# Performance work log

Hardware: AMD Instinct MI355X
Metric: run time of the kernel (lower is better)

## Reference

```python
import jax, jax.numpy as jnp
import numpy as np

B, T, DM, H, D = 2, 4096, 1024, 16, 64
HD = H * D
PHASE_SCALE = 10.0


def _multiscale_phasors(num_heads, head_dim):
    # Deterministic multiscale frequencies: RoPE-like geometric spacing over
    # the feature dim, with a per-head octave scale (reconstruction of the
    # registered buffer `freqs` from generate_multiscale_phasors).
    d = np.arange(head_dim, dtype=np.float32) / head_dim
    base = 10000.0 ** (-d)                      # (D,)
    head_scale = 2.0 ** (-np.arange(num_heads, dtype=np.float32))  # (H,)
    return jnp.asarray(2.0 * np.pi * head_scale[:, None] * base[None, :],
                       dtype=jnp.float32)       # (H, D)


def setup_inputs() -> dict:
    key = jax.random.key(0)
    k0, k1, k2, k3 = jax.random.split(key, 4)
    x = jax.random.normal(k0, (B, T, DM), jnp.float32)
    Wk = jax.random.normal(k1, (DM, HD), jnp.float32) / np.float32(np.sqrt(DM))
    Wv = jax.random.normal(k2, (DM, HD), jnp.float32) / np.float32(np.sqrt(DM))
    Wo = jax.random.normal(k3, (HD, DM), jnp.float32) / np.float32(np.sqrt(HD))
    gate = jnp.full((H, 2), 0.5, jnp.float32)
    freqs = _multiscale_phasors(H, D)
    return {"x": x, "Wk": Wk, "Wv": Wv, "Wo": Wo, "gate": gate, "freqs": freqs}


def _holo_fused_step(v, binder, probe):
    # (cumsum(v * binder, dim=1) * probe).real / sqrt(1..T)
    mem = jnp.cumsum(v * binder, axis=1)                     # (B,T,H,D) complex64
    t = v.shape[1]
    scale = jnp.sqrt(jnp.arange(1, t + 1, dtype=jnp.float32))[None, :, None, None]
    return jnp.real(mem * probe) / scale                     # (B,T,H,D) float32


def reference(x, Wk, Wv, Wo, gate, freqs):
    Bb, Tt, _ = x.shape
    k_real = (x @ Wk).reshape(Bb, Tt, H, D)                  # (B,T,H,D)
    v = (x @ Wv).reshape(Bb, Tt, H, D).astype(jnp.complex64)
    k = jnp.exp(1j * (k_real * PHASE_SCALE))                 # unit phasors, q = k
    # Positional path: rotors = exp(i * t * freqs)
    t = jnp.arange(Tt, dtype=jnp.float32)
    rotors = jnp.exp(1j * (t[:, None, None] * freqs))[None]  # (1,T,H,D)
    out_pos = _holo_fused_step(v, rotors, jnp.conj(rotors))
    # Associative path: bind with conj of shifted keys, retrieve with q=k
    k_shifted = jnp.roll(k, 1, axis=1).at[:, 0].set(0.0)
    out_assoc = _holo_fused_step(v, jnp.conj(k_shifted), k)
    g_pos = gate[:, 0][None, None, :, None]
    g_assoc = gate[:, 1][None, None, :, None]
    out = out_pos * g_pos + out_assoc * g_assoc              # (B,T,H,D)
    return out.reshape(Bb, Tt, HD) @ Wo                      # dropout p=0 -> identity
```

## Files before the change

### kernel.cpp

```cpp
#include <hip/hip_runtime.h>


#define B_ 2
#define T_ 4096
#define H_ 16
#define D_ 64
#define M_ (B_*T_)
#define PHASE_SCALE 10.0f

typedef _Float16 f16;
typedef unsigned int u32;
typedef __attribute__((ext_vector_type(8))) _Float16 f16x8;
typedef __attribute__((ext_vector_type(4))) _Float16 f16x4;
typedef __attribute__((ext_vector_type(4))) float f32x4;


__global__ void k_prep(const float* __restrict__ x, const float* __restrict__ Wk,
                       const float* __restrict__ Wv, const float* __restrict__ Wo,
                       f16* __restrict__ xh, f16* __restrict__ Wkvt, f16* __restrict__ Wot) {
  __shared__ float tile[32][33];
  const int z = blockIdx.z;
  const int tx = threadIdx.x, ty = threadIdx.y;
  if (z == 3) {
    const int blk = blockIdx.y * 32 + blockIdx.x;
    const size_t base = (size_t)blk * 256 + ty * 32 + tx;
    #pragma unroll
    for (int i = 0; i < 8; ++i) {
      size_t idx = (base + (size_t)i * 262144) * 4;
      float4 v = *reinterpret_cast<const float4*>(x + idx);
      f16x4 o; o[0] = (f16)v.x; o[1] = (f16)v.y; o[2] = (f16)v.z; o[3] = (f16)v.w;
      *reinterpret_cast<f16x4*>(xh + idx) = o;
    }
    return;
  }
  const float* src = (z == 0) ? Wk : (z == 1) ? Wv : Wo;
  f16* dst = (z == 0) ? Wkvt : (z == 1) ? (Wkvt + (size_t)1024 * 1024) : Wot;
  const int bx = blockIdx.x, by = blockIdx.y;
  #pragma unroll
  for (int r = 0; r < 32; r += 8)
    tile[ty + r][tx] = src[(size_t)(by * 32 + ty + r) * 1024 + bx * 32 + tx];
  __syncthreads();
  #pragma unroll
  for (int r = 0; r < 32; r += 8)
    dst[(size_t)(bx * 32 + ty + r) * 1024 + by * 32 + tx] = (f16)tile[tx][ty + r];
}


__device__ __forceinline__ void gl2lds16(const f16* g, char* l) {
  __builtin_amdgcn_global_load_lds((const __attribute__((address_space(1))) u32*)g,
                                   (__attribute__((address_space(3))) u32*)l, 16, 0, 0);
}

#define S_BAR() __builtin_amdgcn_s_barrier()
#define WAIT_LGKM0() do { asm volatile("s_waitcnt lgkmcnt(0)" ::: "memory"); \
                          __builtin_amdgcn_sched_barrier(0); } while (0)
#define WAIT_VM(n) asm volatile("s_waitcnt vmcnt(" #n ")" ::: "memory")

#define STAGE_A(gp, ldsoff, kkt) do { \
  gl2lds16((gp) + (size_t)(kkt) * 64, smem + (ldsoff) + tid * 16); \
  if constexpr (MI == 4) \
    gl2lds16((gp) + (size_t)(kkt) * 64 + 64 * 1024, smem + (ldsoff) + 8192 + tid * 16); \
} while (0)
#define STAGE_B(gp, ldsoff, kkt) do { \
  gl2lds16((gp) + (size_t)(kkt) * 64, smem + (ldsoff) + tid * 16); \
  gl2lds16((gp) + (size_t)(kkt) * 64 + 64 * 1024, smem + (ldsoff) + 8192 + tid * 16); \
} while (0)

#define PHASE(AH, BH, READ_A, READ_B, VMW, STG) do { \
  if (READ_A) { \
    _Pragma("unroll") for (int mi = 0; mi < MI; ++mi) \
    _Pragma("unroll") for (int kk = 0; kk < 2; ++kk) \
      aF[mi][kk] = *(const f16x8*)(smem + curbuf + (AH) * AHB + offA[mi][kk]); \
  } \
  if (READ_B) { \
    _Pragma("unroll") for (int nj = 0; nj < 2; ++nj) \
    _Pragma("unroll") for (int kk = 0; kk < 2; ++kk) \
      bF[BH][nj][kk] = *(const f16x8*)(smem + curbuf + 2 * AHB + (BH) * 16384 + offB[nj][kk]); \
  } \
  STG; \
  S_BAR(); \
  WAIT_LGKM0(); \
  __builtin_amdgcn_s_setprio(1); \
  _Pragma("unroll") for (int mi = 0; mi < MI; ++mi) \
  _Pragma("unroll") for (int nj = 0; nj < 2; ++nj) \
  _Pragma("unroll") for (int kk = 0; kk < 2; ++kk) \
    acc[(AH) * 2 + (BH)][mi][nj] = __builtin_amdgcn_mfma_f32_16x16x32_f16( \
        aF[mi][kk], bF[BH][nj][kk], acc[(AH) * 2 + (BH)][mi][nj], 0, 0, 0); \
  __builtin_amdgcn_s_setprio(0); \
  VMW; \
  S_BAR(); \
} while (0)

template<int MI>
__launch_bounds__(512, 1)
__global__ void k_gemm8(const f16* __restrict__ A, const f16* __restrict__ Bt,
                        float* __restrict__ C32, f16* __restrict__ C16) {
  extern __shared__ char smem[];
  constexpr int AH_R = MI * 32;
  constexpr int AHB  = AH_R * 128;
  constexpr int BUFSZ = 2 * AHB + 32768;
  const int tid  = threadIdx.x;
  const int lane = tid & 63;
  const int wid  = tid >> 6;
  const int wr   = wid >> 2, wc = wid & 3;
  const int lr   = lane & 15, hi = lane >> 4;
  const int m0   = blockIdx.x * (MI * 64);
  const int n0   = blockIdx.y * 256;

  const int rsub = tid >> 3;
  const int csw  = ((tid & 7) ^ (rsub & 7)) * 8;
  const f16* gA0 = A  + (size_t)(m0 + rsub) * 1024 + csw;
  const f16* gA1 = gA0 + (size_t)AH_R * 1024;
  const f16* gB0 = Bt + (size_t)(n0 + rsub) * 1024 + csw;
  const f16* gB1 = gB0 + (size_t)128 * 1024;

  int offA[MI][2], offB[2][2];
  #pragma unroll
  for (int mi = 0; mi < MI; ++mi)
    #pragma unroll
    for (int kk = 0; kk < 2; ++kk) {
      int row = wr * (MI * 16) + mi * 16 + lr;
      offA[mi][kk] = row * 128 + (((kk * 4 + hi) ^ (row & 7)) << 4);
    }
  #pragma unroll
  for (int nj = 0; nj < 2; ++nj)
    #pragma unroll
    for (int kk = 0; kk < 2; ++kk) {
      int row = wc * 32 + nj * 16 + lr;
      offB[nj][kk] = row * 128 + (((kk * 4 + hi) ^ (row & 7)) << 4);
    }

  f32x4 acc[4][MI][2] = {};
  f16x8 aF[MI][2], bF[2][2][2];

  STAGE_A(gA0, 0,            0);
  STAGE_B(gB0, 2 * AHB,      0);
  STAGE_A(gA1, AHB,          0);
  STAGE_A(gA0, BUFSZ,        1);
  STAGE_B(gB1, 2 * AHB + 16384, 0);
  STAGE_B(gB0, BUFSZ + 2 * AHB, 1);
  if constexpr (MI == 4) WAIT_VM(8); else WAIT_VM(6);
  S_BAR();

  for (int kt = 0; kt < 14; ++kt) {
    const int curbuf = (kt & 1) * BUFSZ;
    const int nxtbuf = curbuf ^ BUFSZ;
    PHASE(0, 0, 1, 1, if constexpr (MI == 4) WAIT_VM(4); else WAIT_VM(3),
          STAGE_A(gA1, nxtbuf + AHB, kt + 1));
    PHASE(0, 1, 0, 1, (void)0, STAGE_A(gA0, curbuf, kt + 2));
    PHASE(1, 0, 1, 0, (void)0, STAGE_B(gB1, nxtbuf + 2 * AHB + 16384, kt + 1));
    PHASE(1, 1, 0, 0, if constexpr (MI == 4) WAIT_VM(8); else WAIT_VM(6),
          STAGE_B(gB0, curbuf + 2 * AHB, kt + 2));
  }
  {
    const int curbuf = 0, nxtbuf = BUFSZ;
    PHASE(0, 0, 1, 1, if constexpr (MI == 4) WAIT_VM(4); else WAIT_VM(3),
          STAGE_A(gA1, nxtbuf + AHB, 15));
    PHASE(0, 1, 0, 1, (void)0, (void)0);
    PHASE(1, 0, 1, 0, (void)0, STAGE_B(gB1, nxtbuf + 2 * AHB + 16384, 15));
    PHASE(1, 1, 0, 0, if constexpr (MI == 4) WAIT_VM(4); else WAIT_VM(3), (void)0);
  }
  {
    const int curbuf = BUFSZ;
    PHASE(0, 0, 1, 1, WAIT_VM(0), (void)0);
    PHASE(0, 1, 0, 1, (void)0, (void)0);
    PHASE(1, 0, 1, 0, (void)0, (void)0);
    PHASE(1, 1, 0, 0, (void)0, (void)0);
  }

  const int rb = hi * 4;
  #pragma unroll
  for (int ah = 0; ah < 2; ++ah)
    #pragma unroll
    for (int bh = 0; bh < 2; ++bh)
      #pragma unroll
      for (int mi = 0; mi < MI; ++mi)
        #pragma unroll
        for (int nj = 0; nj < 2; ++nj) {
          f32x4 a4 = acc[ah * 2 + bh][mi][nj];
          const int row = m0 + ah * AH_R + wr * (MI * 16) + mi * 16 + rb;
          const int col = n0 + bh * 128 + wc * 32 + nj * 16 + lr;
          if (col < 1024) {
            #pragma unroll
            for (int r = 0; r < 4; ++r)
              C32[(size_t)(row + r) * 1024 + col] = a4[r];
          } else {
            #pragma unroll
            for (int r = 0; r < 4; ++r)
              C16[(size_t)(row + r) * 1024 + (col - 1024)] = (f16)a4[r];
          }
        }
}


__global__ void k_scan_part(const float* __restrict__ kf, const f16* __restrict__ vh,
                            const float* __restrict__ freqs, float4* __restrict__ tot) {
  const int bid = blockIdx.x;
  const int cg = bid & 15;
  const int h  = (bid >> 4) & 15;
  const int b  = bid >> 8;
  const int w  = threadIdx.x >> 6;
  const int d  = threadIdx.x & 63;
  const int c  = cg * 4 + w;
  const int t0 = c * 64;
  const int col = h * 64 + d;
  const float f = freqs[col];

  float bc = 0.f, bs = 0.f;
  if (t0 > 0) {
    float krp = kf[(size_t)(b * T_ + t0 - 1) * 1024 + col];
    __sincosf(PHASE_SCALE * krp, &bs, &bc);
  }
  double rev = (double)t0 * (double)f * 0.15915494309189535;
  rev -= floor(rev);
  float ph = (float)rev * 6.28318530717958647692f;
  float ri, rc; __sincosf(ph, &ri, &rc);
  float sf, cf; __sincosf(f, &sf, &cf);

  float pr = 0.f, pi = 0.f, ar = 0.f, ai = 0.f;
  #pragma unroll 4
  for (int tt = 0; tt < 64; ++tt) {
    size_t row = (size_t)(b * T_ + t0 + tt) * 1024 + col;
    float v  = (float)vh[row];
    float kr = kf[row];
    pr = fmaf(v, rc, pr); pi = fmaf(v, ri, pi);
    ar = fmaf(v, bc, ar); ai = fmaf(-v, bs, ai);
    __sincosf(PHASE_SCALE * kr, &bs, &bc);
    float nrc = rc * cf - ri * sf;
    ri = rc * sf + ri * cf; rc = nrc;
  }
  tot[((size_t)(c * 2 + b) * 16 + h) * 64 + d] = make_float4(pr, pi, ar, ai);
}

__global__ void k_scan_out(const float* __restrict__ kf, const f16* __restrict__ vh,
                           const float* __restrict__ freqs, const float4* __restrict__ tot,
                           const float* __restrict__ gate, f16* __restrict__ y) {
  const int bid = blockIdx.x;
  const int cg = bid & 15;
  const int h  = (bid >> 4) & 15;
  const int b  = bid >> 8;
  const int w  = threadIdx.x >> 6;
  const int d  = threadIdx.x & 63;
  const int c  = cg * 4 + w;
  const int t0 = c * 64;
  const int col = h * 64 + d;
  const float f = freqs[col];
  const float gp = gate[2 * h], ga = gate[2 * h + 1];

  float pr = 0.f, pi = 0.f, ar = 0.f, ai = 0.f;
  for (int cc = 0; cc < c; ++cc) {
    float4 tv = tot[((size_t)(cc * 2 + b) * 16 + h) * 64 + d];
    pr += tv.x; pi += tv.y; ar += tv.z; ai += tv.w;
  }

  float bc = 0.f, bs = 0.f;
  if (t0 > 0) {
    float krp = kf[(size_t)(b * T_ + t0 - 1) * 1024 + col];
    __sincosf(PHASE_SCALE * krp, &bs, &bc);
  }
  double rev = (double)t0 * (double)f * 0.15915494309189535;
  rev -= floor(rev);
  float ph = (float)rev * 6.28318530717958647692f;
  float ri, rc; __sincosf(ph, &ri, &rc);
  float sf, cf; __sincosf(f, &sf, &cf);

  #pragma unroll 4
  for (int tt = 0; tt < 64; ++tt) {
    int t = t0 + tt;
    size_t row = (size_t)(b * T_ + t) * 1024 + col;
    float v  = (float)vh[row];
    float kr = kf[row];
    pr = fmaf(v, rc, pr); pi = fmaf(v, ri, pi);
    ar = fmaf(v, bc, ar); ai = fmaf(-v, bs, ai);
    float kc, ks; __sincosf(PHASE_SCALE * kr, &ks, &kc);
    float inv = rsqrtf((float)(t + 1));
    float op = fmaf(pr, rc, pi * ri) * inv;
    float oa = fmaf(ar, kc, -(ai * ks)) * inv;
    y[row] = (f16)(gp * op + ga * oa);
    bs = ks; bc = kc;
    float nrc = rc * cf - ri * sf;
    ri = rc * sf + ri * cf; rc = nrc;
  }
}


extern "C" void kernel_launch(void* const* d_in, const int* in_sizes, int n_in,
                              void* d_out, int out_size, void* d_ws, size_t ws_size,
                              hipStream_t stream) {
  const float* x     = (const float*)d_in[0];
  const float* Wk    = (const float*)d_in[1];
  const float* Wv    = (const float*)d_in[2];
  const float* Wo    = (const float*)d_in[3];
  const float* gate  = (const float*)d_in[4];
  const float* freqs = (const float*)d_in[5];
  float* out = (float*)d_out;

  char* ws = (char*)d_ws;
  size_t off = 0;
  auto alloc = [&](size_t bytes) { void* p = ws + off; off += (bytes + 255) & ~255ull; return p; };

  f16*    xh   = (f16*)   alloc((size_t)M_ * 1024 * sizeof(f16));
  f16*    Wkvt = (f16*)   alloc((size_t)2048 * 1024 * sizeof(f16));
  f16*    Wot  = (f16*)   alloc((size_t)1024 * 1024 * sizeof(f16));
  float*  kf   = (float*) alloc((size_t)M_ * 1024 * sizeof(float));
  f16*    vh   = (f16*)   alloc((size_t)M_ * 1024 * sizeof(f16));
  float4* tot  = (float4*)alloc((size_t)64 * B_ * H_ * D_ * sizeof(float4));
  f16*    yh   = xh;

  hipFuncSetAttribute(reinterpret_cast<const void*>(&k_gemm8<4>),
                      hipFuncAttributeMaxDynamicSharedMemorySize, 131072);
  hipFuncSetAttribute(reinterpret_cast<const void*>(&k_gemm8<2>),
                      hipFuncAttributeMaxDynamicSharedMemorySize, 98304);

  hipLaunchKernelGGL(k_prep, dim3(32, 32, 4), dim3(32, 8), 0, stream,
                     x, Wk, Wv, Wo, xh, Wkvt, Wot);
  hipLaunchKernelGGL(k_gemm8<4>, dim3(32, 8), dim3(512), 131072, stream, xh, Wkvt, kf, vh);
  hipLaunchKernelGGL(k_scan_part, dim3(512), dim3(256), 0, stream, kf, vh, freqs, tot);
  hipLaunchKernelGGL(k_scan_out,  dim3(512), dim3(256), 0, stream, kf, vh, freqs, tot, gate, yh);
  hipLaunchKernelGGL(k_gemm8<2>, dim3(64, 4), dim3(512), 98304, stream, yh, Wot, out, nullptr);
}
```

Measured before the change: 200.0 us.

## Restructure GEMM pipeline into two phases with fixed 256-row A tiles

Replaces the four-phase-per-k-step GEMM schedule with two phases. The first loads all A and B fragments and computes the top half, and the second reloads A for the bottom half and reuses the B fragments. The M tile is fixed at 256 rows and the N tile is parameterized instead. The output projection now uses 256x128 tiles instead of 128x256. The goal is fewer barriers per k-step and more MFMAs per barrier. In exchange, more fragment registers are held and the phases have coarser granularity.

Result: no change. 200.7 us (+0.4%).

```diff
diff --git a/kernel.cpp b/kernel.cpp
--- a/kernel.cpp
+++ b/kernel.cpp
@@ -56,116 +56,125 @@
                           __builtin_amdgcn_sched_barrier(0); } while (0)
 #define WAIT_VM(n) asm volatile("s_waitcnt vmcnt(" #n ")" ::: "memory")
 
-#define STAGE_A(gp, ldsoff, kkt) do { \
-  gl2lds16((gp) + (size_t)(kkt) * 64, smem + (ldsoff) + tid * 16); \
-  if constexpr (MI == 4) \
+#define STA(gp, ldsoff, kkt) do { \
+  gl2lds16((gp) + (size_t)(kkt) * 64,              smem + (ldsoff) + tid * 16); \
+  gl2lds16((gp) + (size_t)(kkt) * 64 + 64 * 1024,  smem + (ldsoff) + 8192 + tid * 16); \
+} while (0)
+#define STB(gp, ldsoff, kkt) do { \
+  gl2lds16((gp) + (size_t)(kkt) * 64,              smem + (ldsoff) + tid * 16); \
+  if constexpr (NJ == 2) \
     gl2lds16((gp) + (size_t)(kkt) * 64 + 64 * 1024, smem + (ldsoff) + 8192 + tid * 16); \
 } while (0)
-#define STAGE_B(gp, ldsoff, kkt) do { \
-  gl2lds16((gp) + (size_t)(kkt) * 64, smem + (ldsoff) + tid * 16); \
-  gl2lds16((gp) + (size_t)(kkt) * 64 + 64 * 1024, smem + (ldsoff) + 8192 + tid * 16); \
-} while (0)
-
-#define PHASE(AH, BH, READ_A, READ_B, VMW, STG) do { \
-  if (READ_A) { \
-    _Pragma("unroll") for (int mi = 0; mi < MI; ++mi) \
-    _Pragma("unroll") for (int kk = 0; kk < 2; ++kk) \
-      aF[mi][kk] = *(const f16x8*)(smem + curbuf + (AH) * AHB + offA[mi][kk]); \
-  } \
-  if (READ_B) { \
-    _Pragma("unroll") for (int nj = 0; nj < 2; ++nj) \
-    _Pragma("unroll") for (int kk = 0; kk < 2; ++kk) \
-      bF[BH][nj][kk] = *(const f16x8*)(smem + curbuf + 2 * AHB + (BH) * 16384 + offB[nj][kk]); \
-  } \
+
+#define PH0(CUR, STG) do { \
+  _Pragma("unroll") for (int mi = 0; mi < 4; ++mi) \
+  _Pragma("unroll") for (int kk = 0; kk < 2; ++kk) \
+    aF[mi][kk] = *(const f16x8*)(smem + (CUR) + offA[mi][kk]); \
+  _Pragma("unroll") for (int bh = 0; bh < 2; ++bh) \
+  _Pragma("unroll") for (int nj = 0; nj < NJ; ++nj) \
+  _Pragma("unroll") for (int kk = 0; kk < 2; ++kk) \
+    bF[bh][nj][kk] = *(const f16x8*)(smem + (CUR) + OFF_B0 + bh * BHB + offB[nj][kk]); \
   STG; \
   S_BAR(); \
   WAIT_LGKM0(); \
   __builtin_amdgcn_s_setprio(1); \
-  _Pragma("unroll") for (int mi = 0; mi < MI; ++mi) \
-  _Pragma("unroll") for (int nj = 0; nj < 2; ++nj) \
-  _Pragma("unroll") for (int kk = 0; kk < 2; ++kk) \
-    acc[(AH) * 2 + (BH)][mi][nj] = __builtin_amdgcn_mfma_f32_16x16x32_f16( \
-        aF[mi][kk], bF[BH][nj][kk], acc[(AH) * 2 + (BH)][mi][nj], 0, 0, 0); \
+  _Pragma("unroll") for (int bh = 0; bh < 2; ++bh) \
+  _Pragma("unroll") for (int mi = 0; mi < 4; ++mi) \
+  _Pragma("unroll") for (int nj = 0; nj < NJ; ++nj) \
+  _Pragma("unroll") for (int kk = 0; kk < 2; ++kk) \
+    acc[bh][mi][nj] = __builtin_amdgcn_mfma_f32_16x16x32_f16( \
+        aF[mi][kk], bF[bh][nj][kk], acc[bh][mi][nj], 0, 0, 0); \
+  __builtin_amdgcn_s_setprio(0); \
+  S_BAR(); \
+} while (0)
+
+#define PH1(CUR, STG, VMW) do { \
+  _Pragma("unroll") for (int mi = 0; mi < 4; ++mi) \
+  _Pragma("unroll") for (int kk = 0; kk < 2; ++kk) \
+    aF[mi][kk] = *(const f16x8*)(smem + (CUR) + 16384 + offA[mi][kk]); \
+  STG; \
+  S_BAR(); \
+  WAIT_LGKM0(); \
+  __builtin_amdgcn_s_setprio(1); \
+  _Pragma("unroll") for (int bh = 0; bh < 2; ++bh) \
+  _Pragma("unroll") for (int mi = 0; mi < 4; ++mi) \
+  _Pragma("unroll") for (int nj = 0; nj < NJ; ++nj) \
+  _Pragma("unroll") for (int kk = 0; kk < 2; ++kk) \
+    acc[2 + bh][mi][nj] = __builtin_amdgcn_mfma_f32_16x16x32_f16( \
+        aF[mi][kk], bF[bh][nj][kk], acc[2 + bh][mi][nj], 0, 0, 0); \
   __builtin_amdgcn_s_setprio(0); \
   VMW; \
   S_BAR(); \
 } while (0)
 
-template<int MI>
+template<int NJ>
 __launch_bounds__(512, 1)
-__global__ void k_gemm8(const f16* __restrict__ A, const f16* __restrict__ Bt,
-                        float* __restrict__ C32, f16* __restrict__ C16) {
+__global__ void k_gemm2p(const f16* __restrict__ A, const f16* __restrict__ Bt,
+                         float* __restrict__ C32, f16* __restrict__ C16) {
   extern __shared__ char smem[];
-  constexpr int AH_R = MI * 32;
-  constexpr int AHB  = AH_R * 128;
-  constexpr int BUFSZ = 2 * AHB + 32768;
+  constexpr int BHR    = NJ * 64;
+  constexpr int BHB    = BHR * 128;
+  constexpr int OFF_B0 = 32768;
+  constexpr int BUFSZ  = 32768 + 2 * BHB;
   const int tid  = threadIdx.x;
   const int lane = tid & 63;
   const int wid  = tid >> 6;
   const int wr   = wid >> 2, wc = wid & 3;
   const int lr   = lane & 15, hi = lane >> 4;
-  const int m0   = blockIdx.x * (MI * 64);
-  const int n0   = blockIdx.y * 256;
+  const int m0   = blockIdx.x * 256;
+  const int n0   = blockIdx.y * (NJ * 128);
 
   const int rsub = tid >> 3;
   const int csw  = ((tid & 7) ^ (rsub & 7)) * 8;
   const f16* gA0 = A  + (size_t)(m0 + rsub) * 1024 + csw;
-  const f16* gA1 = gA0 + (size_t)AH_R * 1024;
+  const f16* gA1 = gA0 + (size_t)128 * 1024;
   const f16* gB0 = Bt + (size_t)(n0 + rsub) * 1024 + csw;
-  const f16* gB1 = gB0 + (size_t)128 * 1024;
-
-  int offA[MI][2], offB[2][2];
-  #pragma unroll
-  for (int mi = 0; mi < MI; ++mi)
+  const f16* gB1 = gB0 + (size_t)BHR * 1024;
+
+  int offA[4][2], offB[NJ][2];
+  #pragma unroll
+  for (int mi = 0; mi < 4; ++mi)
     #pragma unroll
     for (int kk = 0; kk < 2; ++kk) {
-      int row = wr * (MI * 16) + mi * 16 + lr;
+      int row = wr * 64 + mi * 16 + lr;
       offA[mi][kk] = row * 128 + (((kk * 4 + hi) ^ (row & 7)) << 4);
     }
   #pragma unroll
-  for (int nj = 0; nj < 2; ++nj)
+  for (int nj = 0; nj < NJ; ++nj)
     #pragma unroll
     for (int kk = 0; kk < 2; ++kk) {
-      int row = wc * 32 + nj * 16 + lr;
+      int row = wc * (16 * NJ) + nj * 16 + lr;
       offB[nj][kk] = row * 128 + (((kk * 4 + hi) ^ (row & 7)) << 4);
     }
 
-  f32x4 acc[4][MI][2] = {};
-  f16x8 aF[MI][2], bF[2][2][2];
-
-  STAGE_A(gA0, 0,            0);
-  STAGE_B(gB0, 2 * AHB,      0);
-  STAGE_A(gA1, AHB,          0);
-  STAGE_A(gA0, BUFSZ,        1);
-  STAGE_B(gB1, 2 * AHB + 16384, 0);
-  STAGE_B(gB0, BUFSZ + 2 * AHB, 1);
-  if constexpr (MI == 4) WAIT_VM(8); else WAIT_VM(6);
+  f32x4 acc[4][4][NJ] = {};
+  f16x8 aF[4][2], bF[2][NJ][2];
+
+  STA(gA0, 0,                0);
+  STB(gB0, OFF_B0,           0);
+  STA(gA1, 16384,            0);
+  STB(gB1, OFF_B0 + BHB,     0);
+  STA(gA0, BUFSZ,            1);
+  STB(gB0, BUFSZ + OFF_B0,   1);
+  if constexpr (NJ == 2) WAIT_VM(4); else WAIT_VM(3);
   S_BAR();
 
   for (int kt = 0; kt < 14; ++kt) {
-    const int curbuf = (kt & 1) * BUFSZ;
-    const int nxtbuf = curbuf ^ BUFSZ;
-    PHASE(0, 0, 1, 1, if constexpr (MI == 4) WAIT_VM(4); else WAIT_VM(3),
-          STAGE_A(gA1, nxtbuf + AHB, kt + 1));
-    PHASE(0, 1, 0, 1, (void)0, STAGE_A(gA0, curbuf, kt + 2));
-    PHASE(1, 0, 1, 0, (void)0, STAGE_B(gB1, nxtbuf + 2 * AHB + 16384, kt + 1));
-    PHASE(1, 1, 0, 0, if constexpr (MI == 4) WAIT_VM(8); else WAIT_VM(6),
-          STAGE_B(gB0, curbuf + 2 * AHB, kt + 2));
+    const int cur = (kt & 1) * BUFSZ;
+    const int nxt = cur ^ BUFSZ;
+    PH0(cur, { STA(gA1, nxt + 16384, kt + 1); STB(gB1, nxt + OFF_B0 + BHB, kt + 1); });
+    PH1(cur, { STA(gA0, cur, kt + 2); STB(gB0, cur + OFF_B0, kt + 2); },
+        if constexpr (NJ == 2) WAIT_VM(4); else WAIT_VM(3));
   }
   {
-    const int curbuf = 0, nxtbuf = BUFSZ;
-    PHASE(0, 0, 1, 1, if constexpr (MI == 4) WAIT_VM(4); else WAIT_VM(3),
-          STAGE_A(gA1, nxtbuf + AHB, 15));
-    PHASE(0, 1, 0, 1, (void)0, (void)0);
-    PHASE(1, 0, 1, 0, (void)0, STAGE_B(gB1, nxtbuf + 2 * AHB + 16384, 15));
-    PHASE(1, 1, 0, 0, if constexpr (MI == 4) WAIT_VM(4); else WAIT_VM(3), (void)0);
+    const int cur = 0, nxt = BUFSZ;
+    PH0(cur, { STA(gA1, nxt + 16384, 15); STB(gB1, nxt + OFF_B0 + BHB, 15); });
+    PH1(cur, (void)0, WAIT_VM(0));
   }
   {
-    const int curbuf = BUFSZ;
-    PHASE(0, 0, 1, 1, WAIT_VM(0), (void)0);
-    PHASE(0, 1, 0, 1, (void)0, (void)0);
-    PHASE(1, 0, 1, 0, (void)0, (void)0);
-    PHASE(1, 1, 0, 0, (void)0, (void)0);
+    const int cur = BUFSZ;
+    PH0(cur, (void)0);
+    PH1(cur, (void)0, (void)0);
   }
 
   const int rb = hi * 4;
@@ -174,12 +183,12 @@
     #pragma unroll
     for (int bh = 0; bh < 2; ++bh)
       #pragma unroll
-      for (int mi = 0; mi < MI; ++mi)
+      for (int mi = 0; mi < 4; ++mi)
         #pragma unroll
-        for (int nj = 0; nj < 2; ++nj) {
+        for (int nj = 0; nj < NJ; ++nj) {
           f32x4 a4 = acc[ah * 2 + bh][mi][nj];
-          const int row = m0 + ah * AH_R + wr * (MI * 16) + mi * 16 + rb;
-          const int col = n0 + bh * 128 + wc * 32 + nj * 16 + lr;
+          const int row = m0 + ah * 128 + wr * 64 + mi * 16 + rb;
+          const int col = n0 + bh * (64 * NJ) + wc * (16 * NJ) + nj * 16 + lr;
           if (col < 1024) {
             #pragma unroll
             for (int r = 0; r < 4; ++r)
@@ -307,15 +316,15 @@
   float4* tot  = (float4*)alloc((size_t)64 * B_ * H_ * D_ * sizeof(float4));
   f16*    yh   = xh;
 
-  hipFuncSetAttribute(reinterpret_cast<const void*>(&k_gemm8<4>),
+  hipFuncSetAttribute(reinterpret_cast<const void*>(&k_gemm2p<2>),
                       hipFuncAttributeMaxDynamicSharedMemorySize, 131072);
-  hipFuncSetAttribute(reinterpret_cast<const void*>(&k_gemm8<2>),
+  hipFuncSetAttribute(reinterpret_cast<const void*>(&k_gemm2p<1>),
                       hipFuncAttributeMaxDynamicSharedMemorySize, 98304);
 
   hipLaunchKernelGGL(k_prep, dim3(32, 32, 4), dim3(32, 8), 0, stream,
                      x, Wk, Wv, Wo, xh, Wkvt, Wot);
-  hipLaunchKernelGGL(k_gemm8<4>, dim3(32, 8), dim3(512), 131072, stream, xh, Wkvt, kf, vh);
+  hipLaunchKernelGGL(k_gemm2p<2>, dim3(32, 8), dim3(512), 131072, stream, xh, Wkvt, kf, vh);
   hipLaunchKernelGGL(k_scan_part, dim3(512), dim3(256), 0, stream, kf, vh, freqs, tot);
   hipLaunchKernelGGL(k_scan_out,  dim3(512), dim3(256), 0, stream, kf, vh, freqs, tot, gate, yh);
-  hipLaunchKernelGGL(k_gemm8<2>, dim3(64, 4), dim3(512), 98304, stream, yh, Wot, out, nullptr);
-}
+  hipLaunchKernelGGL(k_gemm2p<1>, dim3(32, 8), dim3(512), 98304, stream, yh, Wot, out, nullptr);
+}
```
